# Kernel tuning notes

Measured on AMD Instinct MI355X. Metric: run time of the kernel, lower is better.

The kernel has to match this reference:

```python
import jax, jax.numpy as jnp
import numpy as np

N = 16384
F_IN = 128
F_OUT = 128


def setup_inputs() -> dict:
    key = jax.random.key(0)
    k1, k2, k3, k4 = jax.random.split(key, 4)
    Adjacency = jax.random.uniform(k1, (N, N), dtype=jnp.float32)
    Features = jax.random.normal(k2, (N, F_IN), dtype=jnp.float32)
    W = jax.random.normal(k3, (F_OUT, F_IN), dtype=jnp.float32) * (1.0 / np.sqrt(F_IN))
    b = jax.random.normal(k4, (F_OUT,), dtype=jnp.float32) * 0.01
    return {"Adjacency": Adjacency, "Features": Features, "W": W, "b": b}


def reference(Adjacency, Features, W, b):
    # normalization = row_sum^{-1/2}, inf (zero-degree) -> 0
    deg = Adjacency.sum(axis=1)                      # [N]
    norm = jnp.where(deg > 0, deg ** -0.5, 0.0)      # [N]
    # A_hat = D^{-1/2} A D^{-1/2}
    A_hat = Adjacency * norm[:, None] * norm[None, :]
    agg = A_hat @ Features                           # [N, F_IN]
    return agg @ W.T + b                             # [N, F_OUT]
```

## Files before the change

kernel.cpp:

```cpp
#include <hip/hip_runtime.h>
#include <stdint.h>

#define NN 16384
#define FD 128

typedef float f32x4 __attribute__((ext_vector_type(4)));
typedef float f32x16 __attribute__((ext_vector_type(16)));
typedef __bf16 bf16x8 __attribute__((ext_vector_type(8)));
typedef unsigned short u16x8 __attribute__((ext_vector_type(8)));
typedef unsigned short u16x4 __attribute__((ext_vector_type(4)));

static __device__ __forceinline__ unsigned short f2bf(float x) {
  return __builtin_bit_cast(unsigned short, (__bf16)x);
}

static __device__ __forceinline__ u16x8 pack8(f32x4 a, f32x4 b) {
  u16x8 r;
  r[0] = f2bf(a.x); r[1] = f2bf(a.y); r[2] = f2bf(a.z); r[3] = f2bf(a.w);
  r[4] = f2bf(b.x); r[5] = f2bf(b.y); r[6] = f2bf(b.z); r[7] = f2bf(b.w);
  return r;
}

static __device__ __forceinline__ u16x4 pack4(f32x4 a) {
  u16x4 r;
  r[0] = f2bf(a.x); r[1] = f2bf(a.y); r[2] = f2bf(a.z); r[3] = f2bf(a.w);
  return r;
}

__global__ __launch_bounds__(256) void k_rownorm(const float* __restrict__ A,
                                                 float* __restrict__ norm) {
  const int row = blockIdx.x;
  const f32x4* ar = (const f32x4*)(A + (size_t)row * NN);
  float s = 0.f;
#pragma unroll 4
  for (int c = threadIdx.x; c < NN / 4; c += 256) {
    f32x4 v = ar[c];
    s += (v.x + v.y) + (v.z + v.w);
  }
#pragma unroll
  for (int off = 32; off > 0; off >>= 1) s += __shfl_xor(s, off, 64);
  __shared__ float red[4];
  const int lane = threadIdx.x & 63, w = threadIdx.x >> 6;
  if (lane == 0) red[w] = s;
  __syncthreads();
  if (threadIdx.x == 0) {
    float d = (red[0] + red[1]) + (red[2] + red[3]);
    norm[row] = d > 0.f ? 1.f / sqrtf(d) : 0.f;
  }
}

__global__ __launch_bounds__(256) void k_fwt(const float* __restrict__ F,
                                             const float* __restrict__ W,
                                             const float* __restrict__ norm,
                                             unsigned short* __restrict__ Bfrag) {
  const int tid = threadIdx.x;
  const int wv = tid >> 6;
  const int l = tid & 63;
  const int lr = l & 31, lg = l >> 5;
  const int j0 = blockIdx.x * 32;

  const float* fp = F + (size_t)(j0 + lr) * FD + lg * 8;
  const float* wp = W + (size_t)(wv * 32 + lr) * FD + lg * 8;

  f32x16 acc;
#pragma unroll
  for (int i = 0; i < 16; ++i) acc[i] = 0.f;

#pragma unroll
  for (int kf = 0; kf < 8; ++kf) {
    f32x4 fa = *(const f32x4*)(fp + kf * 16);
    f32x4 fb = *(const f32x4*)(fp + kf * 16 + 4);
    f32x4 wa = *(const f32x4*)(wp + kf * 16);
    f32x4 wb = *(const f32x4*)(wp + kf * 16 + 4);
    bf16x8 av = __builtin_bit_cast(bf16x8, pack8(fa, fb));
    bf16x8 bv = __builtin_bit_cast(bf16x8, pack8(wa, wb));
    acc = __builtin_amdgcn_mfma_f32_32x32x16_bf16(av, bv, acc, 0, 0, 0);
  }

  const int jt = blockIdx.x * 2;
#pragma unroll
  for (int g = 0; g < 4; ++g) {
    const int jb = j0 + g * 8 + lg * 4;
    u16x4 q;
#pragma unroll
    for (int r2 = 0; r2 < 4; ++r2) q[r2] = f2bf(acc[g * 4 + r2] * norm[jb + r2]);
    const size_t byteoff =
        ((size_t)((jt + (g >> 1)) * 4 + wv) * 64 + (g & 1) * 32 + lr) * 16 +
        lg * 8;
    *(u16x4*)((char*)Bfrag + byteoff) = q;
  }
}

__global__ __launch_bounds__(1024, 4) void k_gcn_gemm(
    const float* __restrict__ A, const unsigned short* __restrict__ Bfrag,
    const float* __restrict__ norm, const float* __restrict__ bias,
    float* __restrict__ out) {
  __shared__ __align__(16) unsigned short Alds[2][64 * 256];

  const int tid = threadIdx.x;
  const int i0 = blockIdx.x * 64;

  const int srow = tid >> 6;
  const int sl = tid & 63;
  const float* aptr = A + (size_t)(i0 + srow) * NN + (size_t)sl * 4;
  const unsigned abase =
      (unsigned)(srow * 512) + ((unsigned)(sl * 8) ^ (unsigned)(srow << 4));

  const int wv = tid >> 6;
  const int c = wv & 3;
  const int m = (wv >> 2) & 1;
  const int kg = wv >> 3;
  const int l = tid & 63;
  const int lr = l & 31, lg = l >> 5;
  const int rowl = m * 32 + lr;
  const unsigned swz = (unsigned)((rowl & 15) << 4);
  const unsigned arb = (unsigned)(rowl * 512);
  const unsigned kgb = (unsigned)(kg * 256);

  const char* bptr = (const char*)Bfrag + (size_t)(c * 64 + l) * 16 +
                     (size_t)kg * 8 * 4096;

  f32x16 acc;
#pragma unroll
  for (int i = 0; i < 16; ++i) acc[i] = 0.f;

  f32x4 a0, a1, a2, a3, b0, b1, b2, b3;

#define ALOAD(RV, S, I)                                                     \
  RV = __builtin_nontemporal_load(                                          \
      (const f32x4*)(aptr + (size_t)(S) * 256 + (size_t)(I) * (16 * NN)));
#define AWRITE(BUF, RV, I)                                                  \
  *(u16x4*)((char*)Alds[BUF] + (abase + (I) * 8192)) = pack4(RV);
#define BARR                                                                \
  do {                                                                      \
    asm volatile("s_waitcnt lgkmcnt(0)" ::: "memory");                      \
    __builtin_amdgcn_s_barrier();                                           \
    __builtin_amdgcn_sched_barrier(0);                                      \
  } while (0)
#define MFMA_BLOCK(CUR, S)                                                  \
  {                                                                         \
    const char* bp_ = bptr + (size_t)(S) * (16 * 4096);                     \
    _Pragma("unroll") for (int kf = 0; kf < 8; ++kf) {                      \
      u16x8 bv = *(const u16x8*)(bp_ + (size_t)kf * 4096);                  \
      unsigned ko = (kgb + (unsigned)(kf * 32) + (unsigned)(lg * 16)) ^ swz;\
      u16x8 av = *(const u16x8*)((const char*)Alds[CUR] + (arb + ko));      \
      acc = __builtin_amdgcn_mfma_f32_32x32x16_bf16(                        \
          __builtin_bit_cast(bf16x8, av), __builtin_bit_cast(bf16x8, bv),   \
          acc, 0, 0, 0);                                                    \
    }                                                                       \
  }

  ALOAD(a0, 0, 0) ALOAD(a1, 0, 1) ALOAD(a2, 0, 2) ALOAD(a3, 0, 3)
  ALOAD(b0, 1, 0) ALOAD(b1, 1, 1) ALOAD(b2, 1, 2) ALOAD(b3, 1, 3)
  AWRITE(0, a0, 0) AWRITE(0, a1, 1) AWRITE(0, a2, 2) AWRITE(0, a3, 3)
  BARR;

#pragma unroll 1
  for (int s = 0; s < 64; s += 2) {
    {
      if (s + 2 < 64) {
        ALOAD(a0, s + 2, 0) ALOAD(a1, s + 2, 1)
        ALOAD(a2, s + 2, 2) ALOAD(a3, s + 2, 3)
      }
      MFMA_BLOCK(0, s)
      AWRITE(1, b0, 0) AWRITE(1, b1, 1) AWRITE(1, b2, 2) AWRITE(1, b3, 3)
      BARR;
    }
    {
      if (s + 3 < 64) {
        ALOAD(b0, s + 3, 0) ALOAD(b1, s + 3, 1)
        ALOAD(b2, s + 3, 2) ALOAD(b3, s + 3, 3)
      }
      MFMA_BLOCK(1, s + 1)
      if (s + 2 < 64) {
        AWRITE(0, a0, 0) AWRITE(0, a1, 1) AWRITE(0, a2, 2) AWRITE(0, a3, 3)
      }
      BARR;
    }
  }
#undef MFMA_BLOCK
#undef BARR
#undef ALOAD
#undef AWRITE

  float* red = (float*)Alds;
  if (kg == 1) {
#pragma unroll
    for (int g = 0; g < 4; ++g) {
      const int jb = m * 32 + g * 8 + lg * 4;
#pragma unroll
      for (int r2 = 0; r2 < 4; ++r2)
        red[(jb + r2) * 128 + c * 32 + lr] = acc[g * 4 + r2];
    }
  }
  __syncthreads();
  if (kg == 0) {
#pragma unroll
    for (int g = 0; g < 4; ++g) {
      const int jb = m * 32 + g * 8 + lg * 4;
#pragma unroll
      for (int r2 = 0; r2 < 4; ++r2)
        red[(jb + r2) * 128 + c * 32 + lr] += acc[g * 4 + r2];
    }
  }
  __syncthreads();

  {
    const int row = tid >> 4;
    const int colseg = (tid & 15) * 8;
    const float nm = norm[i0 + row];
    f32x4 v0 = *(const f32x4*)(red + row * 128 + colseg);
    f32x4 v1 = *(const f32x4*)(red + row * 128 + colseg + 4);
    f32x4 b0v = *(const f32x4*)(bias + colseg);
    f32x4 b1v = *(const f32x4*)(bias + colseg + 4);
    f32x4 o0, o1;
    o0.x = nm * v0.x + b0v.x; o0.y = nm * v0.y + b0v.y;
    o0.z = nm * v0.z + b0v.z; o0.w = nm * v0.w + b0v.w;
    o1.x = nm * v1.x + b1v.x; o1.y = nm * v1.y + b1v.y;
    o1.z = nm * v1.z + b1v.z; o1.w = nm * v1.w + b1v.w;
    float* op = out + (size_t)(i0 + row) * FD + colseg;
    *(f32x4*)op = o0;
    *(f32x4*)(op + 4) = o1;
  }
}

extern "C" void kernel_launch(void* const* d_in, const int* in_sizes, int n_in,
                              void* d_out, int out_size, void* d_ws,
                              size_t ws_size, hipStream_t stream) {
  (void)in_sizes; (void)n_in; (void)out_size; (void)ws_size;
  const float* A = (const float*)d_in[0];
  const float* F = (const float*)d_in[1];
  const float* W = (const float*)d_in[2];
  const float* b = (const float*)d_in[3];
  float* out = (float*)d_out;

  float* norm = (float*)d_ws;
  unsigned short* Bfrag = (unsigned short*)((char*)d_ws + 65536);

  k_rownorm<<<NN, 256, 0, stream>>>(A, norm);
  k_fwt<<<NN / 32, 256, 0, stream>>>(F, W, norm, Bfrag);
  k_gcn_gemm<<<NN / 64, 1024, 0, stream>>>(A, Bfrag, norm, b, out);
}
```

Measured before the change: 395.8 us.

## Fuse row-sum with bf16 swizzled copy of adjacency, GEMM reads via LDS DMA

Adds a path that reads the fp32 adjacency once, computing both the row-degree norm and a bf16 copy stored in a pre-swizzled, tile-ordered image in workspace. The GEMM then streams this half-size image straight into LDS with global_load_lds, with no in-register conversion. This targets the second full fp32 read of A and the conversion work inside the GEMM loop. In exchange it adds a large bf16 image write and reread, so total memory traffic stays about the same, and it needs roughly 512MB of workspace, otherwise the old path runs.

After: 489.0 us. 23.6% more time.

```diff
diff --git a/kernel.cpp b/kernel.cpp
--- a/kernel.cpp
+++ b/kernel.cpp
@@ -26,6 +26,185 @@
   r[0] = f2bf(a.x); r[1] = f2bf(a.y); r[2] = f2bf(a.z); r[3] = f2bf(a.w);
   return r;
 }
+
+static __device__ __forceinline__ void gload_lds16(const void* g, void* l) {
+  __builtin_amdgcn_global_load_lds(
+      (const __attribute__((address_space(1))) unsigned int*)(uintptr_t)g,
+      (__attribute__((address_space(3))) unsigned int*)(unsigned int)(uintptr_t)l,
+      16, 0, 0);
+}
+
+
+__global__ __launch_bounds__(1024) void k_sumcast(
+    const float* __restrict__ A, float* __restrict__ norm,
+    unsigned short* __restrict__ img) {
+  const int tid = threadIdx.x;
+  const int b = blockIdx.x;
+  const int i0 = b * 64;
+  const int rloc = tid >> 4;
+  const int l16 = tid & 15;
+  const float* ar = A + (size_t)(i0 + rloc) * NN + (size_t)l16 * 4;
+  char* ib = (char*)img + (size_t)b * 2097152 + (size_t)rloc * 512;
+  const unsigned kxor = (unsigned)((rloc & 15) << 4);
+  float sx = 0.f, sy = 0.f, sz = 0.f, sw = 0.f;
+#pragma unroll 8
+  for (int i = 0; i < 256; ++i) {
+    f32x4 v = *(const f32x4*)(ar + (size_t)i * 64);
+    sx += v.x; sy += v.y; sz += v.z; sw += v.w;
+    const unsigned kb = (unsigned)(l16 * 8 + (i & 3) * 128) ^ kxor;
+    __builtin_nontemporal_store(
+        pack4(v), (u16x4*)(ib + (size_t)(i >> 2) * 32768 + kb));
+  }
+  float s = (sx + sy) + (sz + sw);
+#pragma unroll
+  for (int off = 8; off > 0; off >>= 1) s += __shfl_xor(s, off, 64);
+  if (l16 == 0) norm[i0 + rloc] = s > 0.f ? 1.f / sqrtf(s) : 0.f;
+}
+
+__global__ __launch_bounds__(1024, 4) void k_gemm_img(
+    const unsigned short* __restrict__ img,
+    const unsigned short* __restrict__ Bfrag, const float* __restrict__ norm,
+    const float* __restrict__ bias, float* __restrict__ out) {
+  __shared__ __align__(16) unsigned short Alds[2][64 * 256];
+
+  const int tid = threadIdx.x;
+  const int b = blockIdx.x;
+  const int i0 = b * 64;
+
+  const int wv = tid >> 6;
+  const int c = wv & 3;
+  const int m = (wv >> 2) & 1;
+  const int kg = wv >> 3;
+  const int l = tid & 63;
+  const int lr = l & 31, lg = l >> 5;
+  const int rowl = m * 32 + lr;
+  const unsigned swz = (unsigned)((rowl & 15) << 4);
+  const unsigned arb = (unsigned)(rowl * 512);
+  const unsigned kgb = (unsigned)(kg * 256);
+
+  const char* isrc = (const char*)img + (size_t)b * 2097152 +
+                     (size_t)wv * 2048 + (size_t)l * 16;
+  const char* bptr = (const char*)Bfrag + (size_t)(c * 64 + l) * 16 +
+                     (size_t)kg * 8 * 4096;
+
+  f32x16 acc;
+#pragma unroll
+  for (int i = 0; i < 16; ++i) acc[i] = 0.f;
+
+#define STAGE(BUF, S)                                                       \
+  {                                                                         \
+    const char* s_ = isrc + (size_t)(S) * 32768;                            \
+    char* d_ = (char*)Alds[BUF] + (size_t)wv * 2048 + (size_t)l * 16;       \
+    gload_lds16(s_, d_);                                                    \
+    gload_lds16(s_ + 1024, d_ + 1024);                                      \
+  }
+#define MFMA_BLOCK(CUR, S)                                                  \
+  {                                                                         \
+    const char* bp_ = bptr + (size_t)(S) * (16 * 4096);                     \
+    _Pragma("unroll") for (int kf = 0; kf < 8; ++kf) {                      \
+      u16x8 bv = *(const u16x8*)(bp_ + (size_t)kf * 4096);                  \
+      unsigned ko = (kgb + (unsigned)(kf * 32) + (unsigned)(lg * 16)) ^ swz;\
+      u16x8 av = *(const u16x8*)((const char*)Alds[CUR] + (arb + ko));      \
+      acc = __builtin_amdgcn_mfma_f32_32x32x16_bf16(                        \
+          __builtin_bit_cast(bf16x8, av), __builtin_bit_cast(bf16x8, bv),   \
+          acc, 0, 0, 0);                                                    \
+    }                                                                       \
+  }
+
+  STAGE(0, 0)
+  __syncthreads();
+#pragma unroll 1
+  for (int s = 0; s < 64; ++s) {
+    const int cur = s & 1;
+    if (s + 1 < 64) STAGE(cur ^ 1, s + 1)
+    MFMA_BLOCK(cur, s)
+    __syncthreads();
+  }
+#undef MFMA_BLOCK
+#undef STAGE
+
+  float* red = (float*)Alds;
+  if (kg == 1) {
+#pragma unroll
+    for (int g = 0; g < 4; ++g) {
+      const int jb = m * 32 + g * 8 + lg * 4;
+#pragma unroll
+      for (int r2 = 0; r2 < 4; ++r2)
+        red[(jb + r2) * 128 + c * 32 + lr] = acc[g * 4 + r2];
+    }
+  }
+  __syncthreads();
+  if (kg == 0) {
+#pragma unroll
+    for (int g = 0; g < 4; ++g) {
+      const int jb = m * 32 + g * 8 + lg * 4;
+#pragma unroll
+      for (int r2 = 0; r2 < 4; ++r2)
+        red[(jb + r2) * 128 + c * 32 + lr] += acc[g * 4 + r2];
+    }
+  }
+  __syncthreads();
+  {
+    const int row = tid >> 4;
+    const int colseg = (tid & 15) * 8;
+    const float nm = norm[i0 + row];
+    f32x4 v0 = *(const f32x4*)(red + row * 128 + colseg);
+    f32x4 v1 = *(const f32x4*)(red + row * 128 + colseg + 4);
+    f32x4 b0v = *(const f32x4*)(bias + colseg);
+    f32x4 b1v = *(const f32x4*)(bias + colseg + 4);
+    f32x4 o0, o1;
+    o0.x = nm * v0.x + b0v.x; o0.y = nm * v0.y + b0v.y;
+    o0.z = nm * v0.z + b0v.z; o0.w = nm * v0.w + b0v.w;
+    o1.x = nm * v1.x + b1v.x; o1.y = nm * v1.y + b1v.y;
+    o1.z = nm * v1.z + b1v.z; o1.w = nm * v1.w + b1v.w;
+    float* op = out + (size_t)(i0 + row) * FD + colseg;
+    *(f32x4*)op = o0;
+    *(f32x4*)(op + 4) = o1;
+  }
+}
+
+__global__ __launch_bounds__(256) void k_fwt(const float* __restrict__ F,
+                                             const float* __restrict__ W,
+                                             const float* __restrict__ norm,
+                                             unsigned short* __restrict__ Bfrag) {
+  const int tid = threadIdx.x;
+  const int wv = tid >> 6;
+  const int l = tid & 63;
+  const int lr = l & 31, lg = l >> 5;
+  const int j0 = blockIdx.x * 32;
+
+  const float* fp = F + (size_t)(j0 + lr) * FD + lg * 8;
+  const float* wp = W + (size_t)(wv * 32 + lr) * FD + lg * 8;
+
+  f32x16 acc;
+#pragma unroll
+  for (int i = 0; i < 16; ++i) acc[i] = 0.f;
+
+#pragma unroll
+  for (int kf = 0; kf < 8; ++kf) {
+    f32x4 fa = *(const f32x4*)(fp + kf * 16);
+    f32x4 fb = *(const f32x4*)(fp + kf * 16 + 4);
+    f32x4 wa = *(const f32x4*)(wp + kf * 16);
+    f32x4 wb = *(const f32x4*)(wp + kf * 16 + 4);
+    bf16x8 av = __builtin_bit_cast(bf16x8, pack8(fa, fb));
+    bf16x8 bv = __builtin_bit_cast(bf16x8, pack8(wa, wb));
+    acc = __builtin_amdgcn_mfma_f32_32x32x16_bf16(av, bv, acc, 0, 0, 0);
+  }
+
+  const int jt = blockIdx.x * 2;
+#pragma unroll
+  for (int g = 0; g < 4; ++g) {
+    const int jb = j0 + g * 8 + lg * 4;
+    u16x4 q;
+#pragma unroll
+    for (int r2 = 0; r2 < 4; ++r2) q[r2] = f2bf(acc[g * 4 + r2] * norm[jb + r2]);
+    const size_t byteoff =
+        ((size_t)((jt + (g >> 1)) * 4 + wv) * 64 + (g & 1) * 32 + lr) * 16 +
+        lg * 8;
+    *(u16x4*)((char*)Bfrag + byteoff) = q;
+  }
+}
+
 
 __global__ __launch_bounds__(256) void k_rownorm(const float* __restrict__ A,
                                                  float* __restrict__ norm) {
@@ -46,48 +225,6 @@
   if (threadIdx.x == 0) {
     float d = (red[0] + red[1]) + (red[2] + red[3]);
     norm[row] = d > 0.f ? 1.f / sqrtf(d) : 0.f;
-  }
-}
-
-__global__ __launch_bounds__(256) void k_fwt(const float* __restrict__ F,
-                                             const float* __restrict__ W,
-                                             const float* __restrict__ norm,
-                                             unsigned short* __restrict__ Bfrag) {
-  const int tid = threadIdx.x;
-  const int wv = tid >> 6;
-  const int l = tid & 63;
-  const int lr = l & 31, lg = l >> 5;
-  const int j0 = blockIdx.x * 32;
-
-  const float* fp = F + (size_t)(j0 + lr) * FD + lg * 8;
-  const float* wp = W + (size_t)(wv * 32 + lr) * FD + lg * 8;
-
-  f32x16 acc;
-#pragma unroll
-  for (int i = 0; i < 16; ++i) acc[i] = 0.f;
-
-#pragma unroll
-  for (int kf = 0; kf < 8; ++kf) {
-    f32x4 fa = *(const f32x4*)(fp + kf * 16);
-    f32x4 fb = *(const f32x4*)(fp + kf * 16 + 4);
-    f32x4 wa = *(const f32x4*)(wp + kf * 16);
-    f32x4 wb = *(const f32x4*)(wp + kf * 16 + 4);
-    bf16x8 av = __builtin_bit_cast(bf16x8, pack8(fa, fb));
-    bf16x8 bv = __builtin_bit_cast(bf16x8, pack8(wa, wb));
-    acc = __builtin_amdgcn_mfma_f32_32x32x16_bf16(av, bv, acc, 0, 0, 0);
-  }
-
-  const int jt = blockIdx.x * 2;
-#pragma unroll
-  for (int g = 0; g < 4; ++g) {
-    const int jb = j0 + g * 8 + lg * 4;
-    u16x4 q;
-#pragma unroll
-    for (int r2 = 0; r2 < 4; ++r2) q[r2] = f2bf(acc[g * 4 + r2] * norm[jb + r2]);
-    const size_t byteoff =
-        ((size_t)((jt + (g >> 1)) * 4 + wv) * 64 + (g & 1) * 32 + lr) * 16 +
-        lg * 8;
-    *(u16x4*)((char*)Bfrag + byteoff) = q;
   }
 }
 
@@ -204,7 +341,6 @@
     }
   }
   __syncthreads();
-
   {
     const int row = tid >> 4;
     const int colseg = (tid & 15) * 8;
@@ -227,7 +363,7 @@
 extern "C" void kernel_launch(void* const* d_in, const int* in_sizes, int n_in,
                               void* d_out, int out_size, void* d_ws,
                               size_t ws_size, hipStream_t stream) {
-  (void)in_sizes; (void)n_in; (void)out_size; (void)ws_size;
+  (void)in_sizes; (void)n_in; (void)out_size;
   const float* A = (const float*)d_in[0];
   const float* F = (const float*)d_in[1];
   const float* W = (const float*)d_in[2];
@@ -237,7 +373,15 @@
   float* norm = (float*)d_ws;
   unsigned short* Bfrag = (unsigned short*)((char*)d_ws + 65536);
 
-  k_rownorm<<<NN, 256, 0, stream>>>(A, norm);
-  k_fwt<<<NN / 32, 256, 0, stream>>>(F, W, norm, Bfrag);
-  k_gcn_gemm<<<NN / 64, 1024, 0, stream>>>(A, Bfrag, norm, b, out);
-}
+  const size_t need = 65536ULL + 4194304ULL + (size_t)NN * NN * 2ULL;
+  if (ws_size >= need) {
+    unsigned short* img = (unsigned short*)((char*)d_ws + 65536 + 4194304);
+    k_sumcast<<<NN / 64, 1024, 0, stream>>>(A, norm, img);
+    k_fwt<<<NN / 32, 256, 0, stream>>>(F, W, norm, Bfrag);
+    k_gemm_img<<<NN / 64, 1024, 0, stream>>>(img, Bfrag, norm, b, out);
+  } else {
+    k_rownorm<<<NN, 256, 0, stream>>>(A, norm);
+    k_fwt<<<NN / 32, 256, 0, stream>>>(F, W, norm, Bfrag);
+    k_gcn_gemm<<<NN / 64, 1024, 0, stream>>>(A, Bfrag, norm, b, out);
+  }
+}
```
